# Optimization experiments

Hardware: AMD Instinct MI355X
Metric: run time of the kernel (lower is better)

The kernel has to match this reference:

```python
import jax, jax.numpy as jnp
import numpy as np


def setup_inputs() -> dict:
    key = jax.random.key(0)
    k1, k2 = jax.random.split(key)
    B, L, D = 8, 2048, 128
    query = jax.random.normal(k1, (B, L, D), dtype=jnp.float32)
    value = jax.random.normal(k2, (B, L, D), dtype=jnp.float32)
    return {"query": query, "value": value}


def reference(query, value):
    # scores: [B, Lq, Lk] = query @ value^T (note: NO 1/sqrt(d) scaling, key == value)
    scores = jnp.einsum("bqd,bkd->bqk", query, value)
    weights = jax.nn.softmax(scores, axis=-1)
    # context: [B, Lq, D]
    context = jnp.einsum("bqk,bkd->bqd", weights, value)
    return context
```

## Files before the change

kernel.cpp:

```cpp
#include <hip/hip_runtime.h>
#include <hip/hip_fp16.h>

typedef _Float16 f16;
typedef __attribute__((ext_vector_type(8))) _Float16 f16x8;
typedef __attribute__((ext_vector_type(4))) _Float16 f16x4;
typedef __attribute__((ext_vector_type(4))) short s16x4;
typedef __attribute__((ext_vector_type(4))) float f32x4;
typedef __attribute__((ext_vector_type(2))) float f32x2;

#define MFMA16(a,b,c) __builtin_amdgcn_mfma_f32_16x16x32_f16(a,b,c,0,0,0)
#define EXP2(x) __builtin_amdgcn_exp2f(x)
#define LOG2E 1.4426950408889634f

#define B_DIM 8
#define L_DIM 2048
#define D_DIM 128
#define NGRP 4
#define KVB 64
#define NTILES 8
#define BLKB 1040
#define TILE_B (16 * BLKB)
#define P_ST 72
#define SLAB_ST 132
#define SMEM_B 137216

__device__ __forceinline__ unsigned ldsa(const void* p) {
    return (unsigned)(unsigned long long)(const __attribute__((address_space(3))) char*)p;
}

#define TRRD(d, a, O) asm volatile("ds_read_b64_tr_b16 %0, %1 offset:" O : "=v"(d) : "v"(a))
#define LGKM0() do { asm volatile("s_waitcnt lgkmcnt(0)" ::: "memory"); __builtin_amdgcn_sched_barrier(0); } while (0)

#define PVND(TL, TH, PA0, PA1, ND) { \
    union { s16x4 s2[2]; f16x8 v; } uu; uu.s2[0] = TL; uu.s2[1] = TH; \
    acc[0][ND] = MFMA16(PA0, uu.v, acc[0][ND]); \
    acc[1][ND] = MFMA16(PA1, uu.v, acc[1][ND]); }

#define PV_HALF(AREG, PA0, PA1, S0,S0b,S1,S1b,S2,S2b,S3,S3b, NDB) { \
    s16x4 t0l,t0h,t1l,t1h,t2l,t2h,t3l,t3h; \
    TRRD(t0l, AREG, S0);  TRRD(t0h, AREG, S0b); \
    TRRD(t1l, AREG, S1);  TRRD(t1h, AREG, S1b); \
    TRRD(t2l, AREG, S2);  TRRD(t2h, AREG, S2b); \
    TRRD(t3l, AREG, S3);  TRRD(t3h, AREG, S3b); \
    LGKM0(); \
    __builtin_amdgcn_s_setprio(1); \
    PVND(t0l, t0h, PA0, PA1, NDB+0); PVND(t1l, t1h, PA0, PA1, NDB+1); \
    PVND(t2l, t2h, PA0, PA1, NDB+2); PVND(t3l, t3h, PA0, PA1, NDB+3); \
    __builtin_amdgcn_s_setprio(0); }

__global__ __launch_bounds__(512, 2) void attn_fwd(
    const float* __restrict__ Q, const float* __restrict__ V, float* __restrict__ Out)
{
    __shared__ __align__(16) char smem[SMEM_B];

    const int tid  = threadIdx.x;
    const int wv   = tid >> 6;
    const int grp  = wv >> 1;
    const int qw   = wv & 1;
    const int lane = tid & 63;
    const int lrow = lane & 15;
    const int g    = lane >> 4;

    const int blk = blockIdx.x;
    const int b   = blk & 7;
    const int q0  = (blk >> 3) * 64;

    char* grpbase = smem + grp * (2 * TILE_B);

    f16x8 qhi[2][4], qlo[2][4];
    {
        const float* qb = Q + ((size_t)b * L_DIM + q0 + qw * 32) * D_DIM;
        #pragma unroll
        for (int q2 = 0; q2 < 2; ++q2) {
            const float* qp = qb + (size_t)(q2 * 16 + lrow) * D_DIM + g * 8;
            #pragma unroll
            for (int dt = 0; dt < 4; ++dt) {
                f32x4 f0 = *(const f32x4*)(qp + dt * 32);
                f32x4 f1 = *(const f32x4*)(qp + dt * 32 + 4);
                #pragma unroll
                for (int i = 0; i < 4; ++i) {
                    float s0 = f0[i] * LOG2E;
                    f16 h0 = (f16)s0;
                    qhi[q2][dt][i] = h0;
                    qlo[q2][dt][i] = (f16)(s0 - (float)h0);
                    float s1 = f1[i] * LOG2E;
                    f16 h1 = (f16)s1;
                    qhi[q2][dt][i + 4] = h1;
                    qlo[q2][dt][i + 4] = (f16)(s1 - (float)h1);
                }
            }
        }
    }

    f32x4 acc[2][8];
    #pragma unroll
    for (int q2 = 0; q2 < 2; ++q2)
        #pragma unroll
        for (int i = 0; i < 8; ++i) acc[q2][i] = (f32x4)0.0f;
    float m_run[2] = { -3.0e38f, -3.0e38f }, l_run[2] = { 0.0f, 0.0f };

    const int kvl = qw * 32 + (lane >> 3);
    const int d4l = lane & 7;
    const int gl_off = kvl * D_DIM + d4l * 4;
    const int wbase = ((kvl >> 2) * BLKB) + ((d4l >> 2) * 128) + (kvl & 3) * 32 + (d4l & 3) * 8;
    const int qkoff = (lrow >> 2) * BLKB + (g >> 1) * 128 + (lrow & 3) * 32 + (g & 1) * 16;

    const float* vb = V + ((size_t)b * L_DIM + grp * (L_DIM / NGRP)) * D_DIM;

    {
        const float* vsrc = vb + gl_off;
        f32x4 ld0[16];
        #pragma unroll
        for (int ith = 0; ith < 4; ++ith)
            #pragma unroll
            for (int itd = 0; itd < 4; ++itd)
                ld0[ith * 4 + itd] = *(const f32x4*)(vsrc + ith * 1024 + itd * 32);
        #pragma unroll
        for (int ith = 0; ith < 4; ++ith)
            #pragma unroll
            for (int itd = 0; itd < 4; ++itd) {
                f32x4 f = ld0[ith * 4 + itd];
                f16x4 hv = { (f16)f[0], (f16)f[1], (f16)f[2], (f16)f[3] };
                *(f16x4*)(grpbase + wbase + ith * (2 * BLKB) + itd * 256) = hv;
            }
    }
    __syncthreads();

    for (int t = 0; t < NTILES; ++t) {
        const int c = t & 1;
        char* cur = grpbase + c * TILE_B;
        char* alt = grpbase + (c ^ 1) * TILE_B;
        const bool hn = (t + 1 < NTILES);
        const float* vnext = vb + (size_t)(t + 1) * KVB * D_DIM + gl_off;

        f32x4 ldA[8], ldB[8];
        if (hn) {
            #pragma unroll
            for (int ith = 0; ith < 2; ++ith)
                #pragma unroll
                for (int itd = 0; itd < 4; ++itd)
                    ldA[ith * 4 + itd] = *(const f32x4*)(vnext + ith * 1024 + itd * 32);
        }

        f32x4 s[2][4];
        #pragma unroll
        for (int q2 = 0; q2 < 2; ++q2)
            #pragma unroll
            for (int nt = 0; nt < 4; ++nt) s[q2][nt] = (f32x4)0.0f;
        __builtin_amdgcn_s_setprio(1);
        #pragma unroll
        for (int nt = 0; nt < 4; ++nt) {
            #pragma unroll
            for (int dt = 0; dt < 4; ++dt) {
                f16x8 a = *(const f16x8*)(cur + qkoff + nt * (4 * BLKB) + dt * 256);
                s[0][nt] = MFMA16(a, qhi[0][dt], s[0][nt]);
                s[0][nt] = MFMA16(a, qlo[0][dt], s[0][nt]);
                s[1][nt] = MFMA16(a, qhi[1][dt], s[1][nt]);
                s[1][nt] = MFMA16(a, qlo[1][dt], s[1][nt]);
            }
        }
        __builtin_amdgcn_s_setprio(0);

        if (hn) {
            #pragma unroll
            for (int ith = 0; ith < 2; ++ith)
                #pragma unroll
                for (int itd = 0; itd < 4; ++itd)
                    ldB[ith * 4 + itd] = *(const f32x4*)(vnext + (ith + 2) * 1024 + itd * 32);
        }

        float pm[2];
        #pragma unroll
        for (int q2 = 0; q2 < 2; ++q2) {
            float tm = s[q2][0][0];
            #pragma unroll
            for (int nt = 0; nt < 4; ++nt)
                #pragma unroll
                for (int r = 0; r < 4; ++r) tm = fmaxf(tm, s[q2][nt][r]);
            tm = fmaxf(tm, __shfl_xor(tm, 16));
            tm = fmaxf(tm, __shfl_xor(tm, 32));
            pm[q2] = tm;
        }
        bool need = (pm[0] > m_run[0] + 11.5f) || (pm[1] > m_run[1] + 11.5f);
        if (__any(need)) {
            float scl[2];
            #pragma unroll
            for (int q2 = 0; q2 < 2; ++q2) {
                float mnew = fmaxf(m_run[q2], pm[q2]);
                scl[q2]  = EXP2(m_run[q2] - mnew);
                m_run[q2] = mnew;
                l_run[q2] *= scl[q2];
            }
            float sr[2][4];
            #pragma unroll
            for (int r = 0; r < 4; ++r) {
                sr[0][r] = __shfl(scl[0], g * 4 + r);
                sr[1][r] = __shfl(scl[1], g * 4 + r);
            }
            #pragma unroll
            for (int q2 = 0; q2 < 2; ++q2)
                #pragma unroll
                for (int nd = 0; nd < 8; ++nd)
                    #pragma unroll
                    for (int r = 0; r < 4; ++r) acc[q2][nd][r] *= sr[q2][r];
        }
        #pragma unroll
        for (int q2 = 0; q2 < 2; ++q2) {
            float ps = 0.0f;
            #pragma unroll
            for (int nt = 0; nt < 4; ++nt)
                #pragma unroll
                for (int r = 0; r < 4; ++r) {
                    float p = EXP2(s[q2][nt][r] - m_run[q2]);
                    s[q2][nt][r] = p;
                    ps += p;
                }
            ps += __shfl_xor(ps, 16);
            ps += __shfl_xor(ps, 32);
            l_run[q2] += ps;
        }

        f16* pls = (f16*)(alt + qw * (8 * BLKB));
        #pragma unroll
        for (int q2 = 0; q2 < 2; ++q2) {
            #pragma unroll
            for (int nt = 0; nt < 4; ++nt) {
                f16x4 w = { (f16)s[q2][nt][0], (f16)s[q2][nt][1],
                            (f16)s[q2][nt][2], (f16)s[q2][nt][3] };
                *(f16x4*)(pls + (size_t)(q2 * 16 + lrow) * P_ST + nt * 16 + g * 4) = w;
            }
        }
        f16x8 pa00, pa01, pa10, pa11;
        pa00 = *(const f16x8*)(pls + (size_t)(lrow) * P_ST + g * 8);
        pa01 = *(const f16x8*)(pls + (size_t)(lrow) * P_ST + 32 + g * 8);
        pa10 = *(const f16x8*)(pls + (size_t)(16 + lrow) * P_ST + g * 8);
        pa11 = *(const f16x8*)(pls + (size_t)(16 + lrow) * P_ST + 32 + g * 8);

        if (hn) {
            #pragma unroll
            for (int ith = 0; ith < 2; ++ith)
                #pragma unroll
                for (int itd = 0; itd < 4; ++itd) {
                    f32x4 f = ldA[ith * 4 + itd];
                    f16x4 hv = { (f16)f[0], (f16)f[1], (f16)f[2], (f16)f[3] };
                    *(f16x4*)(alt + wbase + ith * (2 * BLKB) + itd * 256) = hv;
                }
        }

        unsigned atr0 = ldsa(cur) + (unsigned)(g * (2 * BLKB) + lrow * 8);
        unsigned atr1 = atr0 + (unsigned)(8 * BLKB);
        PV_HALF(atr0, pa00, pa10, "0","1040","128","1168","256","1296","384","1424", 0);
        PV_HALF(atr0, pa00, pa10, "512","1552","640","1680","768","1808","896","1936", 4);
        PV_HALF(atr1, pa01, pa11, "0","1040","128","1168","256","1296","384","1424", 0);
        PV_HALF(atr1, pa01, pa11, "512","1552","640","1680","768","1808","896","1936", 4);

        if (hn) {
            #pragma unroll
            for (int ith = 0; ith < 2; ++ith)
                #pragma unroll
                for (int itd = 0; itd < 4; ++itd) {
                    f32x4 f = ldB[ith * 4 + itd];
                    f16x4 hv = { (f16)f[0], (f16)f[1], (f16)f[2], (f16)f[3] };
                    *(f16x4*)(alt + wbase + (ith + 2) * (2 * BLKB) + itd * 256) = hv;
                }
        }
        __syncthreads();
    }

    float* slab = (float*)smem;
    float* mlp  = (float*)(smem + 8 * 32 * SLAB_ST * 4);
    #pragma unroll
    for (int q2 = 0; q2 < 2; ++q2)
        #pragma unroll
        for (int nd = 0; nd < 8; ++nd)
            #pragma unroll
            for (int r = 0; r < 4; ++r)
                slab[(size_t)(wv * 32 + q2 * 16 + g * 4 + r) * SLAB_ST + nd * 16 + lrow] = acc[q2][nd][r];
    if (g == 0) {
        #pragma unroll
        for (int q2 = 0; q2 < 2; ++q2) {
            mlp[wv * 64 + q2 * 16 + lrow]      = m_run[q2];
            mlp[wv * 64 + 32 + q2 * 16 + lrow] = l_run[q2];
        }
    }
    __syncthreads();

    #pragma unroll
    for (int rr = 0; rr < 8; ++rr) {
        int row = wv * 8 + rr;
        int qws = row >> 5, ql = row & 31;
        float mg[4], M = -3.0e38f;
        #pragma unroll
        for (int gg = 0; gg < 4; ++gg) {
            mg[gg] = mlp[(gg * 2 + qws) * 64 + ql];
            M = fmaxf(M, mg[gg]);
        }
        float L = 0.0f, f[4];
        #pragma unroll
        for (int gg = 0; gg < 4; ++gg) {
            f[gg] = EXP2(mg[gg] - M);
            L += f[gg] * mlp[(gg * 2 + qws) * 64 + 32 + ql];
        }
        float inv = 1.0f / L;
        f32x2 o = { 0.0f, 0.0f };
        #pragma unroll
        for (int gg = 0; gg < 4; ++gg) {
            f32x2 v = *(const f32x2*)&slab[(size_t)((gg * 2 + qws) * 32 + ql) * SLAB_ST + lane * 2];
            o[0] += f[gg] * v[0];
            o[1] += f[gg] * v[1];
        }
        o[0] *= inv; o[1] *= inv;
        *(f32x2*)&Out[((size_t)b * L_DIM + q0 + row) * D_DIM + lane * 2] = o;
    }
}

extern "C" void kernel_launch(void* const* d_in, const int* in_sizes, int n_in,
                              void* d_out, int out_size, void* d_ws, size_t ws_size,
                              hipStream_t stream) {
    const float* Q = (const float*)d_in[0];
    const float* V = (const float*)d_in[1];
    float* Out     = (float*)d_out;
    attn_fwd<<<dim3(B_DIM * (L_DIM / 64)), dim3(512), 0, stream>>>(Q, V, Out);
}
```

Before: 45.08 us.

## Pre-convert V to fp16 tiled layout and stream tiles via global_load_lds

Adds a prep kernel that converts V from fp32 to fp16 once, writing it into a swizzled tile layout in the workspace. The attention kernel then copies each KV tile straight into LDS with global_load_lds DMA, with no register staging and no per-block conversion. This removes the repeated fp32 loads and converts that every query block did on the same V, and halves global read bytes. In exchange it adds a second launch and a workspace round trip, and it drops the LDS row padding (BLKB 1040 to 1024), which may bring back bank conflicts.

```diff
diff --git a/kernel.cpp b/kernel.cpp
--- a/kernel.cpp
+++ b/kernel.cpp
@@ -18,8 +18,7 @@
 #define NGRP 4
 #define KVB 64
 #define NTILES 8
-#define BLKB 1040
-#define TILE_B (16 * BLKB)
+#define TILE_B 16384
 #define P_ST 72
 #define SLAB_ST 132
 #define SMEM_B 137216
@@ -30,6 +29,9 @@
 
 #define TRRD(d, a, O) asm volatile("ds_read_b64_tr_b16 %0, %1 offset:" O : "=v"(d) : "v"(a))
 #define LGKM0() do { asm volatile("s_waitcnt lgkmcnt(0)" ::: "memory"); __builtin_amdgcn_sched_barrier(0); } while (0)
+#define GLDS(gp, lp) __builtin_amdgcn_global_load_lds( \
+    (const __attribute__((address_space(1))) unsigned int*)(gp), \
+    (__attribute__((address_space(3))) unsigned int*)(lp), 16, 0, 0)
 
 #define PVND(TL, TH, PA0, PA1, ND) { \
     union { s16x4 s2[2]; f16x8 v; } uu; uu.s2[0] = TL; uu.s2[1] = TH; \
@@ -48,8 +50,28 @@
     PVND(t2l, t2h, PA0, PA1, NDB+2); PVND(t3l, t3h, PA0, PA1, NDB+3); \
     __builtin_amdgcn_s_setprio(0); }
 
+__global__ __launch_bounds__(256) void prep_v(const float* __restrict__ V, f16* __restrict__ ws) {
+    const int blk = blockIdx.x;
+    const float* src = V + (size_t)blk * (KVB * D_DIM);
+    f16* dst = ws + (size_t)blk * (KVB * D_DIM);
+    const int t = threadIdx.x;
+    #pragma unroll
+    for (int ii = 0; ii < 4; ++ii) {
+        int lin = ii * 256 + t;
+        int kv = lin >> 4, oct = lin & 15;
+        const float* sp = src + kv * D_DIM + oct * 8;
+        f32x4 a = *(const f32x4*)sp;
+        f32x4 b = *(const f32x4*)(sp + 4);
+        int c = (kv >> 2) * 64 + (oct >> 1) * 8 + (kv & 3) * 2 + (oct & 1);
+        union { f16 h[8]; f16x8 v; } u;
+        #pragma unroll
+        for (int k = 0; k < 4; ++k) { u.h[k] = (f16)a[k]; u.h[k + 4] = (f16)b[k]; }
+        *(f16x8*)(dst + (size_t)c * 8) = u.v;
+    }
+}
+
 __global__ __launch_bounds__(512, 2) void attn_fwd(
-    const float* __restrict__ Q, const float* __restrict__ V, float* __restrict__ Out)
+    const float* __restrict__ Q, const f16* __restrict__ ws, float* __restrict__ Out)
 {
     __shared__ __align__(16) char smem[SMEM_B];
 
@@ -99,30 +121,15 @@
         for (int i = 0; i < 8; ++i) acc[q2][i] = (f32x4)0.0f;
     float m_run[2] = { -3.0e38f, -3.0e38f }, l_run[2] = { 0.0f, 0.0f };
 
-    const int kvl = qw * 32 + (lane >> 3);
-    const int d4l = lane & 7;
-    const int gl_off = kvl * D_DIM + d4l * 4;
-    const int wbase = ((kvl >> 2) * BLKB) + ((d4l >> 2) * 128) + (kvl & 3) * 32 + (d4l & 3) * 8;
-    const int qkoff = (lrow >> 2) * BLKB + (g >> 1) * 128 + (lrow & 3) * 32 + (g & 1) * 16;
-
-    const float* vb = V + ((size_t)b * L_DIM + grp * (L_DIM / NGRP)) * D_DIM;
+    const int qkoff = (lrow >> 2) * 1024 + (g >> 1) * 128 + (lrow & 3) * 32 + (g & 1) * 16;
+
+    const f16* wsb = ws + (size_t)b * (32 * KVB * D_DIM);
 
     {
-        const float* vsrc = vb + gl_off;
-        f32x4 ld0[16];
-        #pragma unroll
-        for (int ith = 0; ith < 4; ++ith)
-            #pragma unroll
-            for (int itd = 0; itd < 4; ++itd)
-                ld0[ith * 4 + itd] = *(const f32x4*)(vsrc + ith * 1024 + itd * 32);
-        #pragma unroll
-        for (int ith = 0; ith < 4; ++ith)
-            #pragma unroll
-            for (int itd = 0; itd < 4; ++itd) {
-                f32x4 f = ld0[ith * 4 + itd];
-                f16x4 hv = { (f16)f[0], (f16)f[1], (f16)f[2], (f16)f[3] };
-                *(f16x4*)(grpbase + wbase + ith * (2 * BLKB) + itd * 256) = hv;
-            }
+        const f16* w0 = wsb + (size_t)(grp * 8) * 8192 + (size_t)(qw * 512 + lane) * 8;
+        char* ldst = grpbase + qw * 8192;
+        #pragma unroll
+        for (int i = 0; i < 8; ++i) GLDS(w0 + i * 512, ldst + i * 1024);
     }
     __syncthreads();
 
@@ -130,17 +137,6 @@
         const int c = t & 1;
         char* cur = grpbase + c * TILE_B;
         char* alt = grpbase + (c ^ 1) * TILE_B;
-        const bool hn = (t + 1 < NTILES);
-        const float* vnext = vb + (size_t)(t + 1) * KVB * D_DIM + gl_off;
-
-        f32x4 ldA[8], ldB[8];
-        if (hn) {
-            #pragma unroll
-            for (int ith = 0; ith < 2; ++ith)
-                #pragma unroll
-                for (int itd = 0; itd < 4; ++itd)
-                    ldA[ith * 4 + itd] = *(const f32x4*)(vnext + ith * 1024 + itd * 32);
-        }
 
         f32x4 s[2][4];
         #pragma unroll
@@ -152,7 +148,7 @@
         for (int nt = 0; nt < 4; ++nt) {
             #pragma unroll
             for (int dt = 0; dt < 4; ++dt) {
-                f16x8 a = *(const f16x8*)(cur + qkoff + nt * (4 * BLKB) + dt * 256);
+                f16x8 a = *(const f16x8*)(cur + qkoff + nt * 4096 + dt * 256);
                 s[0][nt] = MFMA16(a, qhi[0][dt], s[0][nt]);
                 s[0][nt] = MFMA16(a, qlo[0][dt], s[0][nt]);
                 s[1][nt] = MFMA16(a, qhi[1][dt], s[1][nt]);
@@ -160,14 +156,6 @@
             }
         }
         __builtin_amdgcn_s_setprio(0);
-
-        if (hn) {
-            #pragma unroll
-            for (int ith = 0; ith < 2; ++ith)
-                #pragma unroll
-                for (int itd = 0; itd < 4; ++itd)
-                    ldB[ith * 4 + itd] = *(const f32x4*)(vnext + (ith + 2) * 1024 + itd * 32);
-        }
 
         float pm[2];
         #pragma unroll
@@ -220,7 +208,7 @@
             l_run[q2] += ps;
         }
 
-        f16* pls = (f16*)(alt + qw * (8 * BLKB));
+        f16* pls = (f16*)(alt + qw * 8192);
         #pragma unroll
         for (int q2 = 0; q2 < 2; ++q2) {
             #pragma unroll
@@ -235,35 +223,22 @@
         pa01 = *(const f16x8*)(pls + (size_t)(lrow) * P_ST + 32 + g * 8);
         pa10 = *(const f16x8*)(pls + (size_t)(16 + lrow) * P_ST + g * 8);
         pa11 = *(const f16x8*)(pls + (size_t)(16 + lrow) * P_ST + 32 + g * 8);
-
-        if (hn) {
-            #pragma unroll
-            for (int ith = 0; ith < 2; ++ith)
-                #pragma unroll
-                for (int itd = 0; itd < 4; ++itd) {
-                    f32x4 f = ldA[ith * 4 + itd];
-                    f16x4 hv = { (f16)f[0], (f16)f[1], (f16)f[2], (f16)f[3] };
-                    *(f16x4*)(alt + wbase + ith * (2 * BLKB) + itd * 256) = hv;
-                }
-        }
-
-        unsigned atr0 = ldsa(cur) + (unsigned)(g * (2 * BLKB) + lrow * 8);
-        unsigned atr1 = atr0 + (unsigned)(8 * BLKB);
-        PV_HALF(atr0, pa00, pa10, "0","1040","128","1168","256","1296","384","1424", 0);
-        PV_HALF(atr0, pa00, pa10, "512","1552","640","1680","768","1808","896","1936", 4);
-        PV_HALF(atr1, pa01, pa11, "0","1040","128","1168","256","1296","384","1424", 0);
-        PV_HALF(atr1, pa01, pa11, "512","1552","640","1680","768","1808","896","1936", 4);
-
-        if (hn) {
-            #pragma unroll
-            for (int ith = 0; ith < 2; ++ith)
-                #pragma unroll
-                for (int itd = 0; itd < 4; ++itd) {
-                    f32x4 f = ldB[ith * 4 + itd];
-                    f16x4 hv = { (f16)f[0], (f16)f[1], (f16)f[2], (f16)f[3] };
-                    *(f16x4*)(alt + wbase + (ith + 2) * (2 * BLKB) + itd * 256) = hv;
-                }
-        }
+        LGKM0();
+
+        if (t + 1 < NTILES) {
+            const f16* wnt = wsb + (size_t)(grp * 8 + t + 1) * 8192 + (size_t)(qw * 512 + lane) * 8;
+            char* ldst = alt + qw * 8192;
+            #pragma unroll
+            for (int i = 0; i < 8; ++i) GLDS(wnt + i * 512, ldst + i * 1024);
+        }
+
+        unsigned atr0 = ldsa(cur) + (unsigned)(g * 2048 + lrow * 8);
+        unsigned atr1 = atr0 + 8192u;
+        PV_HALF(atr0, pa00, pa10, "0","1024","128","1152","256","1280","384","1408", 0);
+        PV_HALF(atr0, pa00, pa10, "512","1536","640","1664","768","1792","896","1920", 4);
+        PV_HALF(atr1, pa01, pa11, "0","1024","128","1152","256","1280","384","1408", 0);
+        PV_HALF(atr1, pa01, pa11, "512","1536","640","1664","768","1792","896","1920", 4);
+
         __syncthreads();
     }
 
@@ -320,5 +295,7 @@
     const float* Q = (const float*)d_in[0];
     const float* V = (const float*)d_in[1];
     float* Out     = (float*)d_out;
-    attn_fwd<<<dim3(B_DIM * (L_DIM / 64)), dim3(512), 0, stream>>>(Q, V, Out);
+    f16* ws        = (f16*)d_ws;
+    prep_v<<<dim3(B_DIM * (L_DIM / KVB)), dim3(256), 0, stream>>>(V, ws);
+    attn_fwd<<<dim3(B_DIM * (L_DIM / 64)), dim3(512), 0, stream>>>(Q, ws, Out);
 }
```

Result: faster. 41.39 us (-8.2%).
